# Optimization experiments

Measured on AMD Instinct MI355X. Metric: run time of the kernel, lower is better.

Reference implementation:

```python
import jax, jax.numpy as jnp
import numpy as np

B, N, M = 2, 4096, 12288
K, SH, H, GK, NC, F = 64, 32, 64, 8, 200, 1


def sph_to_cart(theta, phi):
    st = jnp.sin(theta)
    return jnp.stack([st * jnp.cos(phi), st * jnp.sin(phi), jnp.cos(theta)], axis=-1)


def setup_inputs() -> dict:
    key = jax.random.key(0)
    ks = jax.random.split(key, 16)
    theta = jax.random.uniform(ks[0], (B, N)) * jnp.pi
    phi = jax.random.uniform(ks[1], (B, N)) * 2 * jnp.pi
    feat = jax.random.normal(ks[2], (B, N))
    xxx = jnp.stack([theta, phi, feat], axis=1)  # [B,3,N]
    pt = jax.random.uniform(ks[3], (M,)) * jnp.pi
    pp = jax.random.uniform(ks[4], (M,)) * 2 * jnp.pi
    pix_theta_phi = jnp.stack([pt, pp], axis=1)  # [M,2]
    s = 0.1
    return dict(
        xxx=xxx,
        pix_theta_phi=pix_theta_phi,
        att_w1=jax.random.normal(ks[5], (F + 1, SH)) * s,
        att_b1=jnp.zeros((SH,)),
        att_w2=jax.random.normal(ks[6], (SH, 1)) * s,
        att_b2=jnp.zeros((1,)),
        proj_w=jax.random.normal(ks[7], (F, H)) * s,
        proj_b=jnp.zeros((H,)),
        rel_w=jax.random.normal(ks[8], (3, H, H)) * s,
        rel_b=jnp.zeros((3, H)),
        root_w=jax.random.normal(ks[9], (3, H, H)) * s,
        out_w1=jax.random.normal(ks[10], (H, H)) * s,
        out_b1=jnp.zeros((H,)),
        out_w2=jax.random.normal(ks[11], (H, NC)) * s,
        out_b2=jnp.zeros((NC,)),
    )


def reference(xxx, pix_theta_phi, att_w1, att_b1, att_w2, att_b2, proj_w, proj_b,
              rel_w, rel_b, root_w, out_w1, out_b1, out_w2, out_b2):
    # --- sparse healpix sampler ---
    los_tp = jnp.transpose(xxx[:, :2, :], (0, 2, 1))   # [B,N,2]
    x = xxx[:, 2, :][..., None]                        # [B,N,1]
    r_los = sph_to_cart(los_tp[..., 0], los_tp[..., 1])           # [B,N,3]
    r_pix = sph_to_cart(pix_theta_phi[:, 0], pix_theta_phi[:, 1])  # [M,3]
    cos = jnp.clip(jnp.einsum('bnc,mc->bmn', r_los, r_pix), -1.0, 1.0)  # [B,M,N]
    vals, idx = jax.lax.top_k(cos, K)                  # [B,M,K]
    x_g = jax.vmap(lambda xb, ib: xb[ib])(x, idx)      # [B,M,K,F]
    d = jnp.arccos(jnp.clip(vals, -1.0, 1.0))          # [B,M,K]
    feat = jnp.concatenate([x_g, d[..., None]], axis=-1)  # [B,M,K,F+1]
    logits = jax.nn.relu(feat @ att_w1 + att_b1) @ att_w2 + att_b2  # [B,M,K,1]
    w = jax.nn.softmax(logits[..., 0], axis=-1)        # [B,M,K]
    pooled = jnp.einsum('bmk,bmkf->bmf', w, x_g)       # [B,M,F]
    # --- GNN on healpix grid ---
    h = jax.nn.relu(pooled @ proj_w + proj_b)          # [B,M,H]
    m = r_pix.shape[0]
    sq = jnp.sum(r_pix * r_pix, axis=1)
    d2 = sq[:, None] + sq[None, :] - 2.0 * (r_pix @ r_pix.T)       # [M,M]
    d2 = jnp.where(jnp.eye(m, dtype=bool), jnp.inf, d2)  # loop=False
    _, nbr = jax.lax.top_k(-d2, GK)                    # [M,GK] knn_graph
    for i in range(rel_w.shape[0]):
        agg = h[:, nbr, :].sum(axis=2)                 # sum-aggregate neighbor msgs
        h = jax.nn.relu(agg @ rel_w[i] + rel_b[i] + h @ root_w[i])
    graph_feat = h.mean(axis=1)                        # global_mean_pool -> [B,H]
    out = jax.nn.relu(graph_feat @ out_w1 + out_b1) @ out_w2 + out_b2
    return out
```

## Files before the change

### kernel.cpp

```cpp
#include <hip/hip_runtime.h>
#include <hip/hip_bf16.h>

#define B_ 2
#define N_ 4096
#define M_ 12288
#define K_ 64
#define SH_ 32
#define H_ 64
#define GK_ 8
#define NC_ 200

#define SCAP 288
#define KCAP 240
#define MG_ 0.01f
#define C256_ 81.48733086f

static __device__ __forceinline__ unsigned f2key(float f) {
  unsigned b = __float_as_uint(f);
  return (b & 0x80000000u) ? ~b : (b | 0x80000000u);
}
static __device__ __forceinline__ float key2f(unsigned u) {
  unsigned b = (u & 0x80000000u) ? (u & 0x7fffffffu) : ~u;
  return __uint_as_float(b);
}
static __device__ __forceinline__ unsigned long long shflxor64(unsigned long long x, int m) {
  unsigned lo = (unsigned)x, hi = (unsigned)(x >> 32);
  lo = (unsigned)__shfl_xor((int)lo, m);
  hi = (unsigned)__shfl_xor((int)hi, m);
  return ((unsigned long long)hi << 32) | lo;
}
static __device__ __forceinline__ unsigned long long kpack(float s, int j) {
  return ((unsigned long long)f2key(s) << 14) | (unsigned)(16383 - j);
}
static __device__ __forceinline__ unsigned long long spack(float c, int n) {
  return ((unsigned long long)f2key(c) << 12) | (unsigned)(4095 - n);
}
static __device__ __forceinline__ int thbkt(float th) {
  int b = (int)(th * C256_);
  return b < 0 ? 0 : (b > 255 ? 255 : b);
}
static __device__ __forceinline__ float clamp1(float x) { return fminf(1.f, fmaxf(-1.f, x)); }
static __device__ __forceinline__ float rdlane(float v, int c) {
  return __uint_as_float((unsigned)__builtin_amdgcn_readlane((int)__float_as_uint(v), c));
}

__global__ __launch_bounds__(256) void sentinel_vA(float* out, int n, float val) {
  int t = blockIdx.x * 256 + threadIdx.x;
  if (t < n) out[t] = val;
}

#define THRB_ 6144
#define PREPN_ (M_ + B_*N_ + B_*H_)
#define PREPB_ ((PREPN_ + 255)/256)

__global__ __launch_bounds__(256) void prepthr_vA(
    const float* __restrict__ xxx, const float* __restrict__ pix,
    float4* __restrict__ r_pix, float4* __restrict__ r_los, float* __restrict__ gf,
    float* __restrict__ kthr, float* __restrict__ cthr, unsigned* __restrict__ cnt)
{
  const float PI = 3.14159265358979f;
  if ((int)blockIdx.x < THRB_) {
    int gid  = blockIdx.x*4 + (threadIdx.x >> 6);
    int lane = threadIdx.x & 63;
    int tgt  = (gid >= M_) ? 1 : 0;
    int row  = gid - tgt*M_;
    float thp = pix[2*row];
    float cp = cosf(thp), sp = fmaxf(sinf(thp), 1e-6f);
    float thq = ((float)lane + 0.5f) * (PI/64.f);
    float sq = sinf(thq), cq = cosf(thq);
    float rinv = 1.0f / (sq * sp);
    float At = tgt ? (2.f*PI*PI*192.f/(float)N_) : (2.f*PI*PI*128.f/(float)M_);
    float lo = 1e-3f, hi = 3.1414f;
    for (int it = 0; it < 12; ++it) {
      float al = 0.5f*(lo + hi);
      float ca = cosf(al);
      float arg = clamp1((ca - cq*cp) * rinv);
      float ax = fabsf(arg);
      float ac = sqrtf(fmaxf(0.f, 1.f - ax)) *
                 fmaf(ax, fmaf(ax, fmaf(ax, -0.0187293f, 0.0742610f), -0.2121144f), 1.5707288f);
      ac = (arg < 0.f) ? (PI - ac) : ac;
      float S = ac;
      #pragma unroll
      for (int off = 32; off; off >>= 1) S += __shfl_xor(S, off);
      float A = 2.f * S * (PI/64.f);
      if (A < At) lo = al; else hi = al;
    }
    if (lane == 0) {
      float chv = cosf(hi);
      if (tgt) cthr[row] = chv - 1e-5f;
      else     kthr[row] = 2.f*chv - 1.00002f;
    }
  } else {
    int tid = ((int)blockIdx.x - THRB_)*256 + threadIdx.x;
    if (tid < M_) {
      float th = pix[2*tid], ph = pix[2*tid+1];
      float st = sinf(th);
      float x = st*cosf(ph), y = st*sinf(ph), z = cosf(th);
      r_pix[tid] = make_float4(x, y, z, x*x + y*y + z*z);
      atomicAdd(&cnt[thbkt(th)], 1u);
    }
    int t2 = tid - M_;
    if (t2 >= 0 && t2 < B_*N_) {
      int b = t2 >> 12, n = t2 & (N_-1);
      const float* xb = xxx + b*3*N_;
      float th = xb[n], ph = xb[N_+n], ft = xb[2*N_+n];
      float st = sinf(th);
      r_los[t2] = make_float4(st*cosf(ph), st*sinf(ph), cosf(th), ft);
      atomicAdd(&cnt[256 + b*256 + thbkt(th)], 1u);
    }
    int t3 = tid - M_ - B_*N_;
    if (t3 >= 0 && t3 < B_*H_) gf[t3] = 0.0f;
  }
}

__global__ __launch_bounds__(256) void scan_vA(
    const unsigned* __restrict__ cnt, int* __restrict__ pstart, int* __restrict__ lstart,
    unsigned* __restrict__ pcur, unsigned* __restrict__ lcur)
{
  __shared__ unsigned buf[256];
  const int t = threadIdx.x;
  for (int arr = 0; arr < 3; ++arr) {
    unsigned v = cnt[arr*256 + t];
    buf[t] = v;
    __syncthreads();
    for (int off = 1; off < 256; off <<= 1) {
      unsigned o = (t >= off) ? buf[t - off] : 0u;
      __syncthreads();
      buf[t] += o;
      __syncthreads();
    }
    unsigned incl = buf[t], excl = incl - v;
    if (arr == 0) {
      pstart[t] = (int)excl; if (t == 255) pstart[256] = (int)incl;
      pcur[t] = excl;
    } else {
      int b = arr - 1;
      lstart[b*257 + t] = (int)excl; if (t == 255) lstart[b*257 + 256] = (int)incl;
      lcur[b*256 + t] = excl;
    }
    __syncthreads();
  }
}

__global__ __launch_bounds__(256) void scatter_vA(
    const float* __restrict__ xxx, const float* __restrict__ pix,
    const float4* __restrict__ r_pix, const float4* __restrict__ r_los,
    unsigned* __restrict__ pcur, unsigned* __restrict__ lcur,
    float4* __restrict__ spix, int* __restrict__ sjdx,
    float4* __restrict__ slos, int* __restrict__ sldx)
{
  int tid = blockIdx.x * 256 + threadIdx.x;
  if (tid < M_) {
    int bkt = thbkt(pix[2*tid]);
    unsigned pos = atomicAdd(&pcur[bkt], 1u);
    spix[pos] = r_pix[tid];
    sjdx[pos] = tid;
  } else {
    int t2 = tid - M_;
    if (t2 < B_*N_) {
      int b = t2 >> 12, n = t2 & (N_-1);
      int bkt = thbkt(xxx[b*3*N_ + n]);
      unsigned pos = atomicAdd(&lcur[b*256 + bkt], 1u);
      slos[b*N_ + pos] = r_los[t2];
      sldx[b*N_ + pos] = n;
    }
  }
}

__global__ __launch_bounds__(512) void sampler_vA(
    const float* __restrict__ pix,
    const float4* __restrict__ spix, const int* __restrict__ sjdx,
    const float4* __restrict__ slos, const int* __restrict__ sldx,
    const int* __restrict__ lstart, const float4* __restrict__ r_los,
    const float* __restrict__ cthr,
    const float* __restrict__ aw1, const float* __restrict__ ab1,
    const float* __restrict__ aw2, const float* __restrict__ ab2,
    float* __restrict__ pooled)
{
  __shared__ unsigned long long cKey[16][SCAP];
  __shared__ unsigned long long selKey[16][K_];
  __shared__ unsigned hist[16][64];
  __shared__ int bnd[16][16];

  const int tid = threadIdx.x, wv = tid >> 6, lane = tid & 63;
  const int b  = blockIdx.y;
  const int srow0 = blockIdx.x*16 + wv*2, srow1 = srow0 + 1;
  const int r0 = wv*2, r1 = r0 + 1;
  const int m0 = sjdx[srow0], m1 = sjdx[srow1];
  const float4 p0 = spix[srow0], p1 = spix[srow1];
  const float thp0 = pix[2*m0], thp1 = pix[2*m1];
  float th0 = cthr[m0], th1 = cthr[m1];
  const float inv0 = 63.999f / (1.000001f - th0);
  const float inv1 = 63.999f / (1.000001f - th1);
  const float4* sl = slos + b * N_;
  const int* sx = sldx + b * N_;
  const float4* rl = r_los + b * N_;
  const int* ls = lstart + b * 257;
  const unsigned long long ltm = (1ull << lane) - 1ull;

  hist[r0][lane] = 0u; hist[r1][lane] = 0u;

  unsigned cnt0 = 0, cnt1 = 0;
  {
    float al0 = acosf(clamp1(th0)), al1 = acosf(clamp1(th1));
    int blo = thbkt(fminf(thp0 - al0, thp1 - al1) - MG_);
    int bhi = thbkt(fmaxf(thp0 + al0, thp1 + al1) + MG_);
    int jlo = ls[blo], jhi = ls[bhi + 1];
    for (int base = jlo; base < jhi; base += 64) {
      int pos = base + lane;
      bool act = pos < jhi;
      float c0 = -2.f, c1 = -2.f; int n = 0;
      if (act) {
        float4 v = sl[pos]; n = sx[pos];
        c0 = clamp1(v.x*p0.x + v.y*p0.y + v.z*p0.z);
        c1 = clamp1(v.x*p1.x + v.y*p1.y + v.z*p1.z);
      }
      bool pr0 = c0 > th0, pr1 = c1 > th1;
      unsigned long long mk0 = __ballot(pr0);
      if (mk0) {
        unsigned off = (unsigned)__popcll(mk0 & ltm);
        if (pr0) {
          if (cnt0 + off < SCAP) cKey[r0][cnt0 + off] = spack(c0, n);
          atomicAdd(&hist[r0][(int)((c0 - th0) * inv0)], 1u);
        }
        cnt0 += (unsigned)__popcll(mk0);
      }
      unsigned long long mk1 = __ballot(pr1);
      if (mk1) {
        unsigned off = (unsigned)__popcll(mk1 & ltm);
        if (pr1) {
          if (cnt1 + off < SCAP) cKey[r1][cnt1 + off] = spack(c1, n);
          atomicAdd(&hist[r1][(int)((c1 - th1) * inv1)], 1u);
        }
        cnt1 += (unsigned)__popcll(mk1);
      }
    }
  }

  for (int rr = 0; rr < 2; ++rr) {
    const int r = (rr == 0) ? r0 : r1;
    const int m = (rr == 0) ? m0 : m1;
    const float4 p = (rr == 0) ? p0 : p1;
    const float thp = (rr == 0) ? thp0 : thp1;
    float th = (rr == 0) ? th0 : th1;
    float inv = (rr == 0) ? inv0 : inv1;
    unsigned cn = (rr == 0) ? cnt0 : cnt1;

    int tries = 0;
    while (cn < K_ && tries < 3) {
      th = 1.f - 1.6f*(1.f - th); ++tries;
      float al = acosf(clamp1(th));
      int blo = thbkt(thp - al - MG_), bhi = thbkt(thp + al + MG_);
      int jlo = ls[blo], jhi = ls[bhi + 1];
      cn = 0;
      for (int base = jlo; base < jhi; base += 64) {
        int pos = base + lane;
        bool act = pos < jhi;
        float c = -2.f; int n = 0;
        if (act) {
          float4 v = sl[pos]; n = sx[pos];
          c = clamp1(v.x*p.x + v.y*p.y + v.z*p.z);
        }
        bool pr = c > th;
        unsigned long long mk = __ballot(pr);
        if (mk) {
          unsigned off = (unsigned)__popcll(mk & ltm);
          if (pr && cn + off < SCAP) cKey[r][cn + off] = spack(c, n);
          cn += (unsigned)__popcll(mk);
        }
      }
    }

    if (cn < K_ || cn > SCAP) {
      unsigned long long prev = ~0ull;
      for (int rd = 0; rd < K_; ++rd) {
        unsigned long long best = 0ull;
        for (int i = 0; i < 64; ++i) {
          int n = lane + 64*i;
          float4 v = rl[n];
          float c = clamp1(v.x*p.x + v.y*p.y + v.z*p.z);
          unsigned long long k = spack(c, n);
          if (k < prev && k > best) best = k;
        }
        #pragma unroll
        for (int off = 1; off < 64; off <<= 1) {
          unsigned long long o = shflxor64(best, off);
          best = o > best ? o : best;
        }
        if (lane == 0) selKey[r][rd] = best;
        prev = best;
      }
    } else {
      if (tries > 0) {
        inv = 63.999f / (1.000001f - th);
        hist[r][lane] = 0u;
        for (unsigned base = 0; base < cn; base += 64) {
          unsigned it = base + lane;
          if (it < cn) {
            float c = key2f((unsigned)(cKey[r][it] >> 12));
            atomicAdd(&hist[r][(int)((c - th) * inv)], 1u);
          }
        }
      }
      unsigned g = hist[r][lane], s = g;
      #pragma unroll
      for (int off = 1; off < 64; off <<= 1) {
        unsigned t2 = (unsigned)__shfl_down((int)s, off);
        s += (lane + off < 64) ? t2 : 0u;
      }
      unsigned snext = s - g;
      unsigned packed = (s >= K_ && snext < K_) ? (((unsigned)(lane+1) << 16) | snext) : 0u;
      #pragma unroll
      for (int off = 32; off; off >>= 1) {
        unsigned o = (unsigned)__shfl_xor((int)packed, off);
        packed = packed > o ? packed : o;
      }
      const int t = (int)(packed >> 16) - 1;
      const unsigned chi = packed & 0xFFFFu;
      const unsigned need = K_ - chi;
      unsigned hiC = 0, bdC = 0;
      for (unsigned base = 0; base < cn; base += 64) {
        unsigned it = base + lane;
        bool act = it < cn;
        unsigned long long key = act ? cKey[r][it] : 0ull;
        int bin = -1;
        if (act) bin = (int)((key2f((unsigned)(key >> 12)) - th) * inv);
        bool pHi = act && bin > t;
        bool pBd = act && bin == t;
        unsigned long long mH = __ballot(pHi);
        unsigned offH = (unsigned)__popcll(mH & ltm);
        if (pHi && hiC + offH < K_) selKey[r][hiC + offH] = key;
        hiC += (unsigned)__popcll(mH);
        unsigned long long mB = __ballot(pBd);
        unsigned offB = (unsigned)__popcll(mB & ltm);
        if (pBd && bdC + offB < 16u) bnd[r][bdC + offB] = (int)it;
        bdC += (unsigned)__popcll(mB);
      }
      if (bdC <= 16u) {
        if (lane < (int)bdC) {
          unsigned long long ki = cKey[r][bnd[r][lane]];
          int rank = 0;
          for (int j = 0; j < (int)bdC; ++j) rank += (cKey[r][bnd[r][j]] > ki) ? 1 : 0;
          if ((unsigned)rank < need) selKey[r][chi + rank] = ki;
        }
      } else {
        for (unsigned base = 0; base < cn; base += 64) {
          unsigned it = base + lane;
          if (it < cn) {
            unsigned long long ki = cKey[r][it];
            int bin = (int)((key2f((unsigned)(ki >> 12)) - th) * inv);
            if (bin == t) {
              int rank = 0;
              for (unsigned j = 0; j < cn; ++j) {
                unsigned long long kj = cKey[r][j];
                int bj = (int)((key2f((unsigned)(kj >> 12)) - th) * inv);
                rank += (bj == t && kj > ki) ? 1 : 0;
              }
              if ((unsigned)rank < need) selKey[r][chi + rank] = ki;
            }
          }
        }
      }
    }

    {
      unsigned long long key = selKey[r][lane];
      int n = 4095 - (int)(key & 0xFFFull);
      float c = key2f((unsigned)(key >> 12));
      float xg = rl[n].w;
      float d  = acosf(clamp1(c));
      float acc = ab2[0];
      for (int s2 = 0; s2 < SH_; ++s2)
        acc += fmaxf(xg*aw1[s2] + d*aw1[SH_+s2] + ab1[s2], 0.f) * aw2[s2];
      float mx = acc;
      #pragma unroll
      for (int off = 32; off; off >>= 1) mx = fmaxf(mx, __shfl_xor(mx, off));
      float e = expf(acc - mx);
      float se = e, sxe = e * xg;
      #pragma unroll
      for (int off = 32; off; off >>= 1) { se += __shfl_xor(se, off); sxe += __shfl_xor(sxe, off); }
      if (lane == 0) pooled[b*M_ + m] = sxe / se;
    }
  }
}

__global__ __launch_bounds__(512) void knn_vA(
    const float* __restrict__ pix,
    const float4* __restrict__ spix, const int* __restrict__ sjdx,
    const int* __restrict__ pstart, const float4* __restrict__ r_pix,
    const float* __restrict__ kthr, int* __restrict__ nbr)
{
  __shared__ unsigned long long cKey[16][KCAP];

  const int tid = threadIdx.x, wv = tid >> 6, lane = tid & 63;
  const int lr0 = wv*2;
  const int srow0 = blockIdx.x*16 + lr0, srow1 = srow0 + 1;
  const int i0 = sjdx[srow0], i1 = sjdx[srow1];
  const float4 p0 = spix[srow0], p1 = spix[srow1];
  const float thp0 = pix[2*i0], thp1 = pix[2*i1];
  const float t0 = kthr[i0], t1 = kthr[i1];
  const unsigned long long ltm = (1ull << lane) - 1ull;

  unsigned cnt0 = 0, cnt1 = 0;
  {
    float al0 = acosf(clamp1((t0 + 1.00002f)*0.5f));
    float al1 = acosf(clamp1((t1 + 1.00002f)*0.5f));
    int blo = thbkt(fminf(thp0 - al0, thp1 - al1) - MG_);
    int bhi = thbkt(fmaxf(thp0 + al0, thp1 + al1) + MG_);
    int jlo = pstart[blo], jhi = pstart[bhi + 1];
    for (int base = jlo; base < jhi; base += 64) {
      int pos = base + lane;
      bool act = pos < jhi;
      float s0 = -1e30f, s1 = -1e30f; int j = -1;
      if (act) {
        float4 v = spix[pos]; j = sjdx[pos];
        s0 = 2.f*(p0.x*v.x + p0.y*v.y + p0.z*v.z) - v.w;
        s1 = 2.f*(p1.x*v.x + p1.y*v.y + p1.z*v.z) - v.w;
      }
      bool pr0 = act && (j != i0) && (s0 > t0);
      bool pr1 = act && (j != i1) && (s1 > t1);
      unsigned long long mk0 = __ballot(pr0);
      if (mk0) {
        unsigned off = (unsigned)__popcll(mk0 & ltm);
        if (pr0 && cnt0 + off < KCAP) cKey[lr0][cnt0 + off] = kpack(s0, j);
        cnt0 += (unsigned)__popcll(mk0);
      }
      unsigned long long mk1 = __ballot(pr1);
      if (mk1) {
        unsigned off = (unsigned)__popcll(mk1 & ltm);
        if (pr1 && cnt1 + off < KCAP) cKey[lr0+1][cnt1 + off] = kpack(s1, j);
        cnt1 += (unsigned)__popcll(mk1);
      }
    }
  }

  for (int rr = 0; rr < 2; ++rr) {
    const int lr = lr0 + rr;
    const int i  = (rr == 0) ? i0 : i1;
    const float4 pi = (rr == 0) ? p0 : p1;
    const float thp = (rr == 0) ? thp0 : thp1;
    float th = (rr == 0) ? t0 : t1;
    unsigned cn = (rr == 0) ? cnt0 : cnt1;

    int tries = 0;
    while (cn < (unsigned)GK_ && tries < 3) {
      th = 1.6f*th - 0.6f; ++tries;
      float al = acosf(clamp1((th + 1.00002f)*0.5f));
      int blo = thbkt(thp - al - MG_), bhi = thbkt(thp + al + MG_);
      int jlo = pstart[blo], jhi = pstart[bhi + 1];
      cn = 0;
      for (int base = jlo; base < jhi; base += 64) {
        int pos = base + lane;
        bool act = pos < jhi;
        float s = -1e30f; int j = -1;
        if (act) {
          float4 v = spix[pos]; j = sjdx[pos];
          s = 2.f*(pi.x*v.x + pi.y*v.y + pi.z*v.z) - v.w;
        }
        bool pr = act && (j != i) && (s > th);
        unsigned long long mk = __ballot(pr);
        if (mk) {
          unsigned off = (unsigned)__popcll(mk & ltm);
          if (pr && cn + off < KCAP) cKey[lr][cn + off] = kpack(s, j);
          cn += (unsigned)__popcll(mk);
        }
      }
    }

    if (cn >= (unsigned)GK_ && cn <= (unsigned)KCAP) {
      unsigned long long pk[4];
      #pragma unroll
      for (int t2 = 0; t2 < 4; ++t2) {
        int idx = lane + 64*t2;
        pk[t2] = (idx < (int)cn) ? cKey[lr][idx] : 0ull;
      }
      for (int round = 0; round < GK_; ++round) {
        unsigned long long loc = pk[0]; int lt = 0;
        #pragma unroll
        for (int t2 = 1; t2 < 4; ++t2) if (pk[t2] > loc) { loc = pk[t2]; lt = t2; }
        unsigned long long best = loc;
        #pragma unroll
        for (int off = 1; off < 64; off <<= 1) {
          unsigned long long o = shflxor64(best, off);
          best = o > best ? o : best;
        }
        if (loc == best) {
          #pragma unroll
          for (int t2 = 0; t2 < 4; ++t2) if (t2 == lt) pk[t2] = 0ull;
        }
        if (lane == round) nbr[i*GK_ + round] = 16383 - (int)(best & 16383ull);
      }
    } else {
      unsigned long long prev = ~0ull;
      for (int rd = 0; rd < GK_; ++rd) {
        unsigned long long best = 0ull;
        for (int j = lane; j < M_; j += 64) {
          float4 v = r_pix[j];
          float s = 2.f*(pi.x*v.x + pi.y*v.y + pi.z*v.z) - v.w;
          if (j != i) {
            unsigned long long k = kpack(s, j);
            if (k < prev && k > best) best = k;
          }
        }
        #pragma unroll
        for (int off = 1; off < 64; off <<= 1) {
          unsigned long long o = shflxor64(best, off);
          best = o > best ? o : best;
        }
        if (lane == rd) nbr[i*GK_ + rd] = 16383 - (int)(best & 16383ull);
        prev = best;
      }
    }
  }
}

__global__ __launch_bounds__(256) void gnn1f_vA(
    const float* __restrict__ pooled, float* __restrict__ hout, const int* __restrict__ nbr,
    const float* __restrict__ pw, const float* __restrict__ pb,
    const float* __restrict__ relw, const float* __restrict__ relb,
    const float* __restrict__ rootw)
{
  __shared__ float wrel[H_*H_], wroot[H_*H_];
  const int tid = threadIdx.x;
  #pragma unroll
  for (int q = 0; q < 16; ++q) {
    int idx = tid + 256*q;
    wrel[idx]  = relw[idx];
    wroot[idx] = rootw[idx];
  }
  __syncthreads();

  const int lane = tid & 63;
  const int wave = tid >> 6;
  const int b = blockIdx.y;
  const int m0 = blockIdx.x * 16 + wave * 4;
  const float* pldb = pooled + (size_t)b * M_;
  const float pwl = pw[lane], pbl = pb[lane], rbl = relb[lane];

  float h[4], agg[4], acc[4];
  #pragma unroll
  for (int t = 0; t < 4; ++t) {
    int m = m0 + t;
    float ps = pldb[m];
    h[t] = fmaxf(ps*pwl + pbl, 0.f);
    float a = 0.f;
    #pragma unroll
    for (int k = 0; k < GK_; ++k) {
      int nb = nbr[m*GK_ + k];
      nb = nb < 0 ? 0 : (nb >= M_ ? M_-1 : nb);
      float pn = pldb[nb];
      a += fmaxf(pn*pwl + pbl, 0.f);
    }
    agg[t] = a;
    acc[t] = rbl;
  }
  #pragma unroll
  for (int c = 0; c < H_; ++c) {
    float wr = wrel[c*H_ + lane], wo = wroot[c*H_ + lane];
    #pragma unroll
    for (int t = 0; t < 4; ++t)
      acc[t] += rdlane(agg[t], c) * wr + rdlane(h[t], c) * wo;
  }
  #pragma unroll
  for (int t = 0; t < 4; ++t)
    hout[((size_t)b*M_ + m0 + t)*H_ + lane] = fmaxf(acc[t], 0.f);
}

__global__ __launch_bounds__(256) void gnn_vA(
    const float* __restrict__ hin, float* __restrict__ hout, const int* __restrict__ nbr,
    const float* __restrict__ relw, const float* __restrict__ relb,
    const float* __restrict__ rootw)
{
  __shared__ float wrel[H_*H_], wroot[H_*H_];
  const int tid = threadIdx.x;
  #pragma unroll
  for (int q = 0; q < 16; ++q) {
    int idx = tid + 256*q;
    wrel[idx]  = relw[idx];
    wroot[idx] = rootw[idx];
  }
  __syncthreads();

  const int lane = tid & 63;
  const int wave = tid >> 6;
  const int b = blockIdx.y;
  const int m0 = blockIdx.x * 16 + wave * 4;
  const float* hb = hin + (size_t)b * M_ * H_;
  const float rbl = relb[lane];

  float h[4], agg[4], acc[4];
  #pragma unroll
  for (int t = 0; t < 4; ++t) {
    int m = m0 + t;
    h[t] = hb[m*H_ + lane];
    float a = 0.f;
    #pragma unroll
    for (int k = 0; k < GK_; ++k) {
      int nb = nbr[m*GK_ + k];
      nb = nb < 0 ? 0 : (nb >= M_ ? M_-1 : nb);
      a += hb[nb*H_ + lane];
    }
    agg[t] = a;
    acc[t] = rbl;
  }
  #pragma unroll
  for (int c = 0; c < H_; ++c) {
    float wr = wrel[c*H_ + lane], wo = wroot[c*H_ + lane];
    #pragma unroll
    for (int t = 0; t < 4; ++t)
      acc[t] += rdlane(agg[t], c) * wr + rdlane(h[t], c) * wo;
  }
  #pragma unroll
  for (int t = 0; t < 4; ++t)
    hout[((size_t)b*M_ + m0 + t)*H_ + lane] = fmaxf(acc[t], 0.f);
}

__global__ __launch_bounds__(256) void gnn3r_vA(
    const float* __restrict__ hin, float* __restrict__ gf, const int* __restrict__ nbr,
    const float* __restrict__ relw, const float* __restrict__ relb,
    const float* __restrict__ rootw)
{
  __shared__ float wrel[H_*H_], wroot[H_*H_];
  __shared__ float gacc[H_];
  const int tid = threadIdx.x;
  #pragma unroll
  for (int q = 0; q < 16; ++q) {
    int idx = tid + 256*q;
    wrel[idx]  = relw[idx];
    wroot[idx] = rootw[idx];
  }
  if (tid < H_) gacc[tid] = 0.f;
  __syncthreads();

  const int lane = tid & 63;
  const int wave = tid >> 6;
  const int b = blockIdx.y;
  const int m0 = blockIdx.x * 16 + wave * 4;
  const float* hb = hin + (size_t)b * M_ * H_;
  const float rbl = relb[lane];

  float h[4], agg[4], acc[4];
  #pragma unroll
  for (int t = 0; t < 4; ++t) {
    int m = m0 + t;
    h[t] = hb[m*H_ + lane];
    float a = 0.f;
    #pragma unroll
    for (int k = 0; k < GK_; ++k) {
      int nb = nbr[m*GK_ + k];
      nb = nb < 0 ? 0 : (nb >= M_ ? M_-1 : nb);
      a += hb[nb*H_ + lane];
    }
    agg[t] = a;
    acc[t] = rbl;
  }
  #pragma unroll
  for (int c = 0; c < H_; ++c) {
    float wr = wrel[c*H_ + lane], wo = wroot[c*H_ + lane];
    #pragma unroll
    for (int t = 0; t < 4; ++t)
      acc[t] += rdlane(agg[t], c) * wr + rdlane(h[t], c) * wo;
  }
  float ps = fmaxf(acc[0], 0.f) + fmaxf(acc[1], 0.f) + fmaxf(acc[2], 0.f) + fmaxf(acc[3], 0.f);
  atomicAdd(&gacc[lane], ps);
  __syncthreads();
  if (tid < H_) atomicAdd(&gf[b*H_ + tid], gacc[tid]);
}

__global__ __launch_bounds__(256) void head_vA(
    const float* __restrict__ gf, const float* __restrict__ w1,
    const float* __restrict__ b1, const float* __restrict__ w2,
    const float* __restrict__ b2, float* __restrict__ out)
{
  __shared__ float gfm[B_][H_], hid[B_][H_];
  const int tid = threadIdx.x;
  if (tid < B_*H_) gfm[tid >> 6][tid & 63] = gf[tid] * (1.f / (float)M_);
  __syncthreads();
  if (tid < B_*H_) {
    int b = tid >> 6, j = tid & 63;
    float acc = b1[j];
    for (int c = 0; c < H_; ++c) acc += gfm[b][c] * w1[c*H_ + j];
    hid[b][j] = fmaxf(acc, 0.f);
  }
  __syncthreads();
  for (int t = tid; t < B_*NC_; t += 256) {
    int b = t / NC_, o = t - b*NC_;
    float acc = b2[o];
    for (int j = 0; j < H_; ++j) acc += hid[b][j] * w2[j*NC_ + o];
    out[t] = acc;
  }
}

extern "C" void kernel_launch(void* const* d_in, const int* in_sizes, int n_in,
                              void* d_out, int out_size, void* d_ws, size_t ws_size,
                              hipStream_t stream)
{
  float* out = (float*)d_out;

  const size_t need = (size_t)M_*16 + (size_t)B_*N_*16 + (size_t)B_*M_*4
                    + (size_t)M_*GK_*4 + 2*(size_t)B_*M_*H_*4 + (size_t)B_*H_*4;
  bool ok_ws = ws_size >= need;
  bool ok_in = (n_in == 15) && (out_size == B_*NC_)
            && in_sizes[0] == B_*3*N_ && in_sizes[1] == M_*2
            && in_sizes[2] == 2*SH_ && in_sizes[5] == 1
            && in_sizes[8] == 3*H_*H_ && in_sizes[13] == H_*NC_;
  if (!ok_ws || !ok_in) {
    sentinel_vA<<<(out_size + 255)/256, 256, 0, stream>>>(out, out_size, ok_in ? 42.f : 43.f);
    return;
  }

  const float* xxx    = (const float*)d_in[0];
  const float* pix    = (const float*)d_in[1];
  const float* att_w1 = (const float*)d_in[2];
  const float* att_b1 = (const float*)d_in[3];
  const float* att_w2 = (const float*)d_in[4];
  const float* att_b2 = (const float*)d_in[5];
  const float* proj_w = (const float*)d_in[6];
  const float* proj_b = (const float*)d_in[7];
  const float* rel_w  = (const float*)d_in[8];
  const float* rel_b  = (const float*)d_in[9];
  const float* root_w = (const float*)d_in[10];
  const float* out_w1 = (const float*)d_in[11];
  const float* out_b1 = (const float*)d_in[12];
  const float* out_w2 = (const float*)d_in[13];
  const float* out_b2 = (const float*)d_in[14];

  char* w = (char*)d_ws;
  float4* r_pix = (float4*)w;  w += (size_t)M_ * 16;
  float4* r_los = (float4*)w;  w += (size_t)B_ * N_ * 16;
  float*  pooled = (float*)w;  w += (size_t)B_ * M_ * 4;
  int*    nbr = (int*)w;       w += (size_t)M_ * GK_ * 4;
  float*  h0 = (float*)w;      w += (size_t)B_ * M_ * H_ * 4;
  float*  h1 = (float*)w;      w += (size_t)B_ * M_ * H_ * 4;
  float*  gf = (float*)w;      w += (size_t)B_ * H_ * 4;

  float*  kthr = h0;
  float*  cthr = h0 + M_;
  float4* spix = (float4*)(h0 + 2*M_);
  int*    sjdx = (int*)(h0 + 6*M_);
  float4* slos = (float4*)(h0 + 7*M_);
  int*    sldx = (int*)(h0 + 7*M_ + 4*B_*N_);
  unsigned* cnt = (unsigned*)(h0 + 7*M_ + 5*B_*N_);
  int*    pstart = (int*)(cnt + 768);
  int*    lstart = pstart + 257;
  unsigned* pcur = (unsigned*)(lstart + 514);
  unsigned* lcur = pcur + 256;

  hipMemsetAsync(cnt, 0, 768*sizeof(unsigned), stream);
  prepthr_vA<<<THRB_ + PREPB_, 256, 0, stream>>>(xxx, pix, r_pix, r_los, gf, kthr, cthr, cnt);
  scan_vA<<<1, 256, 0, stream>>>(cnt, pstart, lstart, pcur, lcur);
  scatter_vA<<<(M_ + B_*N_ + 255)/256, 256, 0, stream>>>(xxx, pix, r_pix, r_los, pcur, lcur,
                                                         spix, sjdx, slos, sldx);
  sampler_vA<<<dim3(M_/16, B_), 512, 0, stream>>>(pix, spix, sjdx, slos, sldx, lstart, r_los,
                                                  cthr, att_w1, att_b1, att_w2, att_b2, pooled);
  knn_vA<<<M_/16, 512, 0, stream>>>(pix, spix, sjdx, pstart, r_pix, kthr, nbr);
  gnn1f_vA<<<dim3(M_/16, B_), 256, 0, stream>>>(pooled, h1, nbr, proj_w, proj_b,
                                                rel_w + 0*H_*H_, rel_b + 0*H_, root_w + 0*H_*H_);
  gnn_vA<<<dim3(M_/16, B_), 256, 0, stream>>>(h1, h0, nbr, rel_w + 1*H_*H_, rel_b + 1*H_, root_w + 1*H_*H_);
  gnn3r_vA<<<dim3(M_/16, B_), 256, 0, stream>>>(h0, gf, nbr, rel_w + 2*H_*H_, rel_b + 2*H_, root_w + 2*H_*H_);
  head_vA<<<1, 256, 0, stream>>>(gf, out_w1, out_b1, out_w2, out_b2, out);
}
```

Baseline: 275.3 us.

## Replace shared candidate buffer with histogram pass plus recompute pass in sampler

The sampler no longer stores every above-threshold candidate key in a large shared array. It first builds only the histogram and count, then rescans the LOS window and recomputes the dot products, writing high-bin keys directly to the selection buffer and boundary-bin keys to a small buffer for ranking. This cuts shared memory per block (dropping the 16x288 64-bit array), which may raise occupancy. The cost is a second global read pass over the candidate window and recomputed dot products, and when the boundary bin overflows the smaller buffer it falls back to the slow 64-round argmax selection.

```diff
diff --git a/kernel.cpp b/kernel.cpp
--- a/kernel.cpp
+++ b/kernel.cpp
@@ -10,8 +10,8 @@
 #define GK_ 8
 #define NC_ 200
 
-#define SCAP 288
 #define KCAP 240
+#define BCAP2 48
 #define MG_ 0.01f
 #define C256_ 81.48733086f
 
@@ -44,7 +44,7 @@
   return __uint_as_float((unsigned)__builtin_amdgcn_readlane((int)__float_as_uint(v), c));
 }
 
-__global__ __launch_bounds__(256) void sentinel_vA(float* out, int n, float val) {
+__global__ __launch_bounds__(256) void sentinel_vC(float* out, int n, float val) {
   int t = blockIdx.x * 256 + threadIdx.x;
   if (t < n) out[t] = val;
 }
@@ -53,7 +53,7 @@
 #define PREPN_ (M_ + B_*N_ + B_*H_)
 #define PREPB_ ((PREPN_ + 255)/256)
 
-__global__ __launch_bounds__(256) void prepthr_vA(
+__global__ __launch_bounds__(256) void prepthr_vC(
     const float* __restrict__ xxx, const float* __restrict__ pix,
     float4* __restrict__ r_pix, float4* __restrict__ r_los, float* __restrict__ gf,
     float* __restrict__ kthr, float* __restrict__ cthr, unsigned* __restrict__ cnt)
@@ -113,7 +113,7 @@
   }
 }
 
-__global__ __launch_bounds__(256) void scan_vA(
+__global__ __launch_bounds__(256) void scan_vC(
     const unsigned* __restrict__ cnt, int* __restrict__ pstart, int* __restrict__ lstart,
     unsigned* __restrict__ pcur, unsigned* __restrict__ lcur)
 {
@@ -142,7 +142,7 @@
   }
 }
 
-__global__ __launch_bounds__(256) void scatter_vA(
+__global__ __launch_bounds__(256) void scatter_vC(
     const float* __restrict__ xxx, const float* __restrict__ pix,
     const float4* __restrict__ r_pix, const float4* __restrict__ r_los,
     unsigned* __restrict__ pcur, unsigned* __restrict__ lcur,
@@ -167,7 +167,7 @@
   }
 }
 
-__global__ __launch_bounds__(512) void sampler_vA(
+__global__ __launch_bounds__(512) void sampler_vC(
     const float* __restrict__ pix,
     const float4* __restrict__ spix, const int* __restrict__ sjdx,
     const float4* __restrict__ slos, const int* __restrict__ sldx,
@@ -177,10 +177,9 @@
     const float* __restrict__ aw2, const float* __restrict__ ab2,
     float* __restrict__ pooled)
 {
-  __shared__ unsigned long long cKey[16][SCAP];
   __shared__ unsigned long long selKey[16][K_];
+  __shared__ unsigned long long bndK[16][BCAP2];
   __shared__ unsigned hist[16][64];
-  __shared__ int bnd[16][16];
 
   const int tid = threadIdx.x, wv = tid >> 6, lane = tid & 63;
   const int b  = blockIdx.y;
@@ -200,41 +199,29 @@
 
   hist[r0][lane] = 0u; hist[r1][lane] = 0u;
 
-  unsigned cnt0 = 0, cnt1 = 0;
+  int jlo, jhi;
   {
     float al0 = acosf(clamp1(th0)), al1 = acosf(clamp1(th1));
     int blo = thbkt(fminf(thp0 - al0, thp1 - al1) - MG_);
     int bhi = thbkt(fmaxf(thp0 + al0, thp1 + al1) + MG_);
-    int jlo = ls[blo], jhi = ls[bhi + 1];
-    for (int base = jlo; base < jhi; base += 64) {
-      int pos = base + lane;
-      bool act = pos < jhi;
-      float c0 = -2.f, c1 = -2.f; int n = 0;
-      if (act) {
-        float4 v = sl[pos]; n = sx[pos];
-        c0 = clamp1(v.x*p0.x + v.y*p0.y + v.z*p0.z);
-        c1 = clamp1(v.x*p1.x + v.y*p1.y + v.z*p1.z);
-      }
-      bool pr0 = c0 > th0, pr1 = c1 > th1;
-      unsigned long long mk0 = __ballot(pr0);
-      if (mk0) {
-        unsigned off = (unsigned)__popcll(mk0 & ltm);
-        if (pr0) {
-          if (cnt0 + off < SCAP) cKey[r0][cnt0 + off] = spack(c0, n);
-          atomicAdd(&hist[r0][(int)((c0 - th0) * inv0)], 1u);
-        }
-        cnt0 += (unsigned)__popcll(mk0);
-      }
-      unsigned long long mk1 = __ballot(pr1);
-      if (mk1) {
-        unsigned off = (unsigned)__popcll(mk1 & ltm);
-        if (pr1) {
-          if (cnt1 + off < SCAP) cKey[r1][cnt1 + off] = spack(c1, n);
-          atomicAdd(&hist[r1][(int)((c1 - th1) * inv1)], 1u);
-        }
-        cnt1 += (unsigned)__popcll(mk1);
-      }
-    }
+    jlo = ls[blo]; jhi = ls[bhi + 1];
+  }
+
+  unsigned cnt0 = 0, cnt1 = 0;
+  for (int base = jlo; base < jhi; base += 64) {
+    int pos = base + lane;
+    bool act = pos < jhi;
+    float c0 = -2.f, c1 = -2.f;
+    if (act) {
+      float4 v = sl[pos];
+      c0 = clamp1(v.x*p0.x + v.y*p0.y + v.z*p0.z);
+      c1 = clamp1(v.x*p1.x + v.y*p1.y + v.z*p1.z);
+    }
+    bool pr0 = c0 > th0, pr1 = c1 > th1;
+    if (pr0) atomicAdd(&hist[r0][(int)((c0 - th0) * inv0)], 1u);
+    if (pr1) atomicAdd(&hist[r1][(int)((c1 - th1) * inv1)], 1u);
+    cnt0 += (unsigned)__popcll(__ballot(pr0));
+    cnt1 += (unsigned)__popcll(__ballot(pr1));
   }
 
   for (int rr = 0; rr < 2; ++rr) {
@@ -245,33 +232,83 @@
     float th = (rr == 0) ? th0 : th1;
     float inv = (rr == 0) ? inv0 : inv1;
     unsigned cn = (rr == 0) ? cnt0 : cnt1;
+    int wlo = jlo, whi = jhi;
 
     int tries = 0;
     while (cn < K_ && tries < 3) {
       th = 1.f - 1.6f*(1.f - th); ++tries;
+      inv = 63.999f / (1.000001f - th);
       float al = acosf(clamp1(th));
       int blo = thbkt(thp - al - MG_), bhi = thbkt(thp + al + MG_);
-      int jlo = ls[blo], jhi = ls[bhi + 1];
+      wlo = ls[blo]; whi = ls[bhi + 1];
+      hist[r][lane] = 0u;
       cn = 0;
-      for (int base = jlo; base < jhi; base += 64) {
+      for (int base = wlo; base < whi; base += 64) {
         int pos = base + lane;
-        bool act = pos < jhi;
+        bool act = pos < whi;
+        float c = -2.f;
+        if (act) {
+          float4 v = sl[pos];
+          c = clamp1(v.x*p.x + v.y*p.y + v.z*p.z);
+        }
+        bool pr = c > th;
+        if (pr) atomicAdd(&hist[r][(int)((c - th) * inv)], 1u);
+        cn += (unsigned)__popcll(__ballot(pr));
+      }
+    }
+
+    bool done = false;
+    if (cn >= K_) {
+      unsigned g = hist[r][lane], s = g;
+      #pragma unroll
+      for (int off = 1; off < 64; off <<= 1) {
+        unsigned t2 = (unsigned)__shfl_down((int)s, off);
+        s += (lane + off < 64) ? t2 : 0u;
+      }
+      unsigned snext = s - g;
+      unsigned packed = (s >= K_ && snext < K_) ? (((unsigned)(lane+1) << 16) | snext) : 0u;
+      #pragma unroll
+      for (int off = 32; off; off >>= 1) {
+        unsigned o = (unsigned)__shfl_xor((int)packed, off);
+        packed = packed > o ? packed : o;
+      }
+      const int t = (int)(packed >> 16) - 1;
+      const unsigned chi = packed & 0xFFFFu;
+      const unsigned need = K_ - chi;
+
+      unsigned hiC = 0, bdC = 0;
+      for (int base = wlo; base < whi; base += 64) {
+        int pos = base + lane;
+        bool act = pos < whi;
         float c = -2.f; int n = 0;
         if (act) {
           float4 v = sl[pos]; n = sx[pos];
           c = clamp1(v.x*p.x + v.y*p.y + v.z*p.z);
         }
-        bool pr = c > th;
-        unsigned long long mk = __ballot(pr);
-        if (mk) {
-          unsigned off = (unsigned)__popcll(mk & ltm);
-          if (pr && cn + off < SCAP) cKey[r][cn + off] = spack(c, n);
-          cn += (unsigned)__popcll(mk);
-        }
-      }
-    }
-
-    if (cn < K_ || cn > SCAP) {
+        int bin = (act && c > th) ? (int)((c - th) * inv) : -1;
+        bool pHi = bin > t;
+        bool pBd = bin == t;
+        unsigned long long mH = __ballot(pHi);
+        unsigned offH = (unsigned)__popcll(mH & ltm);
+        if (pHi && hiC + offH < K_) selKey[r][hiC + offH] = spack(c, n);
+        hiC += (unsigned)__popcll(mH);
+        unsigned long long mB = __ballot(pBd);
+        unsigned offB = (unsigned)__popcll(mB & ltm);
+        if (pBd && bdC + offB < BCAP2) bndK[r][bdC + offB] = spack(c, n);
+        bdC += (unsigned)__popcll(mB);
+      }
+      if (bdC <= (unsigned)BCAP2) {
+        if (lane < (int)bdC) {
+          unsigned long long ki = bndK[r][lane];
+          int rank = 0;
+          for (int j = 0; j < (int)bdC; ++j) rank += (bndK[r][j] > ki) ? 1 : 0;
+          if ((unsigned)rank < need) selKey[r][chi + rank] = ki;
+        }
+        done = true;
+      }
+    }
+
+    if (!done) {
       unsigned long long prev = ~0ull;
       for (int rd = 0; rd < K_; ++rd) {
         unsigned long long best = 0ull;
@@ -289,77 +326,6 @@
         }
         if (lane == 0) selKey[r][rd] = best;
         prev = best;
-      }
-    } else {
-      if (tries > 0) {
-        inv = 63.999f / (1.000001f - th);
-        hist[r][lane] = 0u;
-        for (unsigned base = 0; base < cn; base += 64) {
-          unsigned it = base + lane;
-          if (it < cn) {
-            float c = key2f((unsigned)(cKey[r][it] >> 12));
-            atomicAdd(&hist[r][(int)((c - th) * inv)], 1u);
-          }
-        }
-      }
-      unsigned g = hist[r][lane], s = g;
-      #pragma unroll
-      for (int off = 1; off < 64; off <<= 1) {
-        unsigned t2 = (unsigned)__shfl_down((int)s, off);
-        s += (lane + off < 64) ? t2 : 0u;
-      }
-      unsigned snext = s - g;
-      unsigned packed = (s >= K_ && snext < K_) ? (((unsigned)(lane+1) << 16) | snext) : 0u;
-      #pragma unroll
-      for (int off = 32; off; off >>= 1) {
-        unsigned o = (unsigned)__shfl_xor((int)packed, off);
-        packed = packed > o ? packed : o;
-      }
-      const int t = (int)(packed >> 16) - 1;
-      const unsigned chi = packed & 0xFFFFu;
-      const unsigned need = K_ - chi;
-      unsigned hiC = 0, bdC = 0;
-      for (unsigned base = 0; base < cn; base += 64) {
-        unsigned it = base + lane;
-        bool act = it < cn;
-        unsigned long long key = act ? cKey[r][it] : 0ull;
-        int bin = -1;
-        if (act) bin = (int)((key2f((unsigned)(key >> 12)) - th) * inv);
-        bool pHi = act && bin > t;
-        bool pBd = act && bin == t;
-        unsigned long long mH = __ballot(pHi);
-        unsigned offH = (unsigned)__popcll(mH & ltm);
-        if (pHi && hiC + offH < K_) selKey[r][hiC + offH] = key;
-        hiC += (unsigned)__popcll(mH);
-        unsigned long long mB = __ballot(pBd);
-        unsigned offB = (unsigned)__popcll(mB & ltm);
-        if (pBd && bdC + offB < 16u) bnd[r][bdC + offB] = (int)it;
-        bdC += (unsigned)__popcll(mB);
-      }
-      if (bdC <= 16u) {
-        if (lane < (int)bdC) {
-          unsigned long long ki = cKey[r][bnd[r][lane]];
-          int rank = 0;
-          for (int j = 0; j < (int)bdC; ++j) rank += (cKey[r][bnd[r][j]] > ki) ? 1 : 0;
-          if ((unsigned)rank < need) selKey[r][chi + rank] = ki;
-        }
-      } else {
-        for (unsigned base = 0; base < cn; base += 64) {
-          unsigned it = base + lane;
-          if (it < cn) {
-            unsigned long long ki = cKey[r][it];
-            int bin = (int)((key2f((unsigned)(ki >> 12)) - th) * inv);
-            if (bin == t) {
-              int rank = 0;
-              for (unsigned j = 0; j < cn; ++j) {
-                unsigned long long kj = cKey[r][j];
-                int bj = (int)((key2f((unsigned)(kj >> 12)) - th) * inv);
-                rank += (bj == t && kj > ki) ? 1 : 0;
-              }
-              if ((unsigned)rank < need) selKey[r][chi + rank] = ki;
-            }
-          }
-        }
       }
     }
 
@@ -384,7 +350,7 @@
   }
 }
 
-__global__ __launch_bounds__(512) void knn_vA(
+__global__ __launch_bounds__(512) void knn_vC(
     const float* __restrict__ pix,
     const float4* __restrict__ spix, const int* __restrict__ sjdx,
     const int* __restrict__ pstart, const float4* __restrict__ r_pix,
@@ -514,7 +480,7 @@
   }
 }
 
-__global__ __launch_bounds__(256) void gnn1f_vA(
+__global__ __launch_bounds__(256) void gnn1f_vC(
     const float* __restrict__ pooled, float* __restrict__ hout, const int* __restrict__ nbr,
     const float* __restrict__ pw, const float* __restrict__ pb,
     const float* __restrict__ relw, const float* __restrict__ relb,
@@ -566,7 +532,7 @@
     hout[((size_t)b*M_ + m0 + t)*H_ + lane] = fmaxf(acc[t], 0.f);
 }
 
-__global__ __launch_bounds__(256) void gnn_vA(
+__global__ __launch_bounds__(256) void gnn_vC(
     const float* __restrict__ hin, float* __restrict__ hout, const int* __restrict__ nbr,
     const float* __restrict__ relw, const float* __restrict__ relb,
     const float* __restrict__ rootw)
@@ -615,7 +581,7 @@
     hout[((size_t)b*M_ + m0 + t)*H_ + lane] = fmaxf(acc[t], 0.f);
 }
 
-__global__ __launch_bounds__(256) void gnn3r_vA(
+__global__ __launch_bounds__(256) void gnn3r_vC(
     const float* __restrict__ hin, float* __restrict__ gf, const int* __restrict__ nbr,
     const float* __restrict__ relw, const float* __restrict__ relb,
     const float* __restrict__ rootw)
@@ -667,7 +633,7 @@
   if (tid < H_) atomicAdd(&gf[b*H_ + tid], gacc[tid]);
 }
 
-__global__ __launch_bounds__(256) void head_vA(
+__global__ __launch_bounds__(256) void head_vC(
     const float* __restrict__ gf, const float* __restrict__ w1,
     const float* __restrict__ b1, const float* __restrict__ w2,
     const float* __restrict__ b2, float* __restrict__ out)
@@ -705,7 +671,7 @@
             && in_sizes[2] == 2*SH_ && in_sizes[5] == 1
             && in_sizes[8] == 3*H_*H_ && in_sizes[13] == H_*NC_;
   if (!ok_ws || !ok_in) {
-    sentinel_vA<<<(out_size + 255)/256, 256, 0, stream>>>(out, out_size, ok_in ? 42.f : 43.f);
+    sentinel_vC<<<(out_size + 255)/256, 256, 0, stream>>>(out, out_size, ok_in ? 42.f : 43.f);
     return;
   }
 
@@ -747,16 +713,16 @@
   unsigned* lcur = pcur + 256;
 
   hipMemsetAsync(cnt, 0, 768*sizeof(unsigned), stream);
-  prepthr_vA<<<THRB_ + PREPB_, 256, 0, stream>>>(xxx, pix, r_pix, r_los, gf, kthr, cthr, cnt);
-  scan_vA<<<1, 256, 0, stream>>>(cnt, pstart, lstart, pcur, lcur);
-  scatter_vA<<<(M_ + B_*N_ + 255)/256, 256, 0, stream>>>(xxx, pix, r_pix, r_los, pcur, lcur,
+  prepthr_vC<<<THRB_ + PREPB_, 256, 0, stream>>>(xxx, pix, r_pix, r_los, gf, kthr, cthr, cnt);
+  scan_vC<<<1, 256, 0, stream>>>(cnt, pstart, lstart, pcur, lcur);
+  scatter_vC<<<(M_ + B_*N_ + 255)/256, 256, 0, stream>>>(xxx, pix, r_pix, r_los, pcur, lcur,
                                                          spix, sjdx, slos, sldx);
-  sampler_vA<<<dim3(M_/16, B_), 512, 0, stream>>>(pix, spix, sjdx, slos, sldx, lstart, r_los,
+  sampler_vC<<<dim3(M_/16, B_), 512, 0, stream>>>(pix, spix, sjdx, slos, sldx, lstart, r_los,
                                                   cthr, att_w1, att_b1, att_w2, att_b2, pooled);
-  knn_vA<<<M_/16, 512, 0, stream>>>(pix, spix, sjdx, pstart, r_pix, kthr, nbr);
-  gnn1f_vA<<<dim3(M_/16, B_), 256, 0, stream>>>(pooled, h1, nbr, proj_w, proj_b,
+  knn_vC<<<M_/16, 512, 0, stream>>>(pix, spix, sjdx, pstart, r_pix, kthr, nbr);
+  gnn1f_vC<<<dim3(M_/16, B_), 256, 0, stream>>>(pooled, h1, nbr, proj_w, proj_b,
                                                 rel_w + 0*H_*H_, rel_b + 0*H_, root_w + 0*H_*H_);
-  gnn_vA<<<dim3(M_/16, B_), 256, 0, stream>>>(h1, h0, nbr, rel_w + 1*H_*H_, rel_b + 1*H_, root_w + 1*H_*H_);
-  gnn3r_vA<<<dim3(M_/16, B_), 256, 0, stream>>>(h0, gf, nbr, rel_w + 2*H_*H_, rel_b + 2*H_, root_w + 2*H_*H_);
-  head_vA<<<1, 256, 0, stream>>>(gf, out_w1, out_b1, out_w2, out_b2, out);
-}
+  gnn_vC<<<dim3(M_/16, B_), 256, 0, stream>>>(h1, h0, nbr, rel_w + 1*H_*H_, rel_b + 1*H_, root_w + 1*H_*H_);
+  gnn3r_vC<<<dim3(M_/16, B_), 256, 0, stream>>>(h0, gf, nbr, rel_w + 2*H_*H_, rel_b + 2*H_, root_w + 2*H_*H_);
+  head_vC<<<1, 256, 0, stream>>>(gf, out_w1, out_b1, out_w2, out_b2, out);
+}
```

Measured after the change: 287.6 us. 4.5% more time.
